# Kernel optimization log

Measured on AMD Instinct MI355X. Metric: run time of the kernel, lower is better.

Reference implementation:

```python
import jax, jax.numpy as jnp
import numpy as np

N = 100000      # nodes
D = 128         # input feature dim
K = 8           # propagation hops (concat K+1 blocks)
HID = 512
OUT = 32
E = 1600000     # edges (avg degree 16)
BN_EPS = 1e-5
DEG_EPS = 1e-8


def setup_inputs() -> dict:
    key = jax.random.key(0)
    ks = jax.random.split(key, 8)
    feature = jax.random.normal(ks[0], (N, D), dtype=jnp.float32)
    coor = jax.random.uniform(ks[1], (N, 2), dtype=jnp.float32)
    edge_index = jax.random.randint(ks[2], (2, E), 0, N, dtype=jnp.int32)
    theta = jnp.array(1.0, dtype=jnp.float32)  # Gaussian bandwidth param
    fan1 = D * (K + 1)
    W1 = jax.random.normal(ks[3], (HID, fan1), dtype=jnp.float32) * (1.0 / np.sqrt(fan1))
    b1 = jnp.zeros((HID,), dtype=jnp.float32)
    gamma = jnp.ones((HID,), dtype=jnp.float32)
    beta = jnp.zeros((HID,), dtype=jnp.float32)
    W2 = jax.random.normal(ks[4], (OUT, HID), dtype=jnp.float32) * (1.0 / np.sqrt(HID))
    b2 = jnp.zeros((OUT,), dtype=jnp.float32)
    return {"feature": feature, "coor": coor, "theta": theta,
            "W1": W1, "b1": b1, "gamma": gamma, "beta": beta,
            "W2": W2, "b2": b2, "edge_index": edge_index, "m": 1}


def reference(feature, coor, theta, W1, b1, gamma, beta, W2, b2, edge_index, m):
    row, col = edge_index[0], edge_index[1]  # dst, src
    # Gaussian kernel edge weights from coordinate distances (gather on coor)
    diff = coor[row] - coor[col]                       # [E, 2]
    dist2 = jnp.sum(diff * diff, axis=-1)              # [E]
    w = jnp.exp(-dist2 * theta / m)                    # [E]
    # degree (row) normalization via scatter-add
    deg = jax.ops.segment_sum(w, row, num_segments=N)  # [N]
    norm = w / (deg[row] + DEG_EPS)                    # [E]
    # K sequential propagations, concat with input (-> N x D*(K+1))
    xs = [feature]
    x = feature
    for _ in range(K):
        msgs = x[col] * norm[:, None]                  # [E, D] gather + weight
        x = jax.ops.segment_sum(msgs, row, num_segments=N)  # [N, D] scatter
        xs.append(x)
    h = jnp.concatenate(xs, axis=-1)                   # [N, D*(K+1)]
    # MLP head: fc1 -> leaky_relu(0.2) -> BatchNorm1d (batch stats) -> fc2
    h = jax.nn.leaky_relu(h @ W1.T + b1, negative_slope=0.2)
    mu = jnp.mean(h, axis=0)
    var = jnp.var(h, axis=0)
    h = (h - mu) * jax.lax.rsqrt(var + BN_EPS) * gamma + beta
    # dropout omitted (deterministic/eval reference)
    return h @ W2.T + b2
```

## Files before the change

### kernel.cpp

```cpp
#include <hip/hip_runtime.h>
#include <hip/hip_bf16.h>
#include <cstdint>
#include <cstddef>

#define NNODES 100000
#define DFEAT 128
#define KHOP 8
#define FAN1 1152
#define HIDN 512
#define OUTD 32
#define NEDGE 1600000
#define BN_EPS 1e-5f
#define DEG_EPS 1e-8f
#define FIXSCALE 67108864.0f

using short8 = __attribute__((ext_vector_type(8))) short;
using f32x4  = __attribute__((ext_vector_type(4))) float;

__device__ __forceinline__ float bf16lo(uint32_t u) { return __uint_as_float(u << 16); }
__device__ __forceinline__ float bf16hi(uint32_t u) { return __uint_as_float(u & 0xffff0000u); }
__device__ __forceinline__ float bf16s(short x) {
    return __uint_as_float(((uint32_t)(uint16_t)x) << 16);
}
__device__ __forceinline__ uint32_t packbf(float a, float b) {
    uint32_t lo = __bfloat16_as_ushort(__float2bfloat16(a));
    uint32_t hi = __bfloat16_as_ushort(__float2bfloat16(b));
    return lo | (hi << 16);
}

__device__ __forceinline__ void gload16(const void* g, void* l) {
    __builtin_amdgcn_global_load_lds(
        (const __attribute__((address_space(1))) uint32_t*)g,
        (__attribute__((address_space(3))) uint32_t*)l, 16, 0, 0);
}

struct Blk3 { const __hip_bfloat16* p[3]; };

__global__ __launch_bounds__(256) void edge_kernel(
    const int* __restrict__ ei, const float* __restrict__ coor,
    const float* __restrict__ theta, const int* __restrict__ mm,
    unsigned long long* __restrict__ packed, unsigned short* __restrict__ rank)
{
    int e = blockIdx.x * 256 + threadIdx.x;
    if (e >= NEDGE) return;
    float tom = theta[0] / (float)mm[0];
    int r = ei[e], c = ei[NEDGE + e];
    float2 pr = *(const float2*)(coor + 2*(size_t)r);
    float2 pc = *(const float2*)(coor + 2*(size_t)c);
    float dx = pr.x - pc.x, dy = pr.y - pc.y;
    float w = expf(-(dx*dx + dy*dy) * tom);
    unsigned long long enc = (1ULL << 48)
        | (unsigned long long)(unsigned int)__float2uint_rn(w * FIXSCALE);
    unsigned long long old = atomicAdd(&packed[r], enc);
    rank[e] = (unsigned short)(old >> 48);
}

__global__ __launch_bounds__(1024) void scan_local(
    const unsigned long long* __restrict__ packed, int* __restrict__ row_ptr,
    int* __restrict__ bsum, int n)
{
    __shared__ int wsum[16];
    int b = blockIdx.x, tid = threadIdx.x;
    int i = b * 1024 + tid;
    int lane = tid & 63, wv = tid >> 6;
    int v = (i < n) ? (int)(packed[i] >> 48) : 0;
    #pragma unroll
    for (int off = 1; off < 64; off <<= 1) {
        int t = __shfl_up(v, off, 64);
        if (lane >= off) v += t;
    }
    if (lane == 63) wsum[wv] = v;
    __syncthreads();
    if (tid < 16) {
        int t = wsum[tid];
        #pragma unroll
        for (int off = 1; off < 16; off <<= 1) {
            int u = __shfl_up(t, off, 64);
            if (tid >= off) t += u;
        }
        wsum[tid] = t;
    }
    __syncthreads();
    int incl = v + ((wv == 0) ? 0 : wsum[wv - 1]);
    if (i < n) row_ptr[i + 1] = incl;
    if (tid == 0) bsum[b] = wsum[15];
}

__global__ __launch_bounds__(128) void scan_carry(int* __restrict__ bsum, int n)
{
    __shared__ int ws[2];
    int tid = threadIdx.x, lane = tid & 63, wv = tid >> 6;
    int v = (tid < n) ? bsum[tid] : 0;
    int incl = v;
    #pragma unroll
    for (int off = 1; off < 64; off <<= 1) {
        int t = __shfl_up(incl, off, 64);
        if (lane >= off) incl += t;
    }
    if (lane == 63) ws[wv] = incl;
    __syncthreads();
    int excl = incl - v + ((wv == 0) ? 0 : ws[0]);
    if (tid < n) bsum[tid] = excl;
}

__global__ __launch_bounds__(256) void scan_add(
    const int* __restrict__ bsum, int* __restrict__ row_ptr, int n)
{
    int i = blockIdx.x * 256 + threadIdx.x;
    if (i == 0) row_ptr[0] = 0;
    if (i < n) row_ptr[i + 1] += bsum[i >> 10];
}

__global__ __launch_bounds__(256) void fill_kernel(
    const int* __restrict__ ei, const float* __restrict__ coor,
    const float* __restrict__ theta, const int* __restrict__ mm,
    const unsigned long long* __restrict__ packed,
    const unsigned short* __restrict__ rank, const int* __restrict__ row_ptr,
    uint2* __restrict__ edat)
{
    int e = blockIdx.x * 256 + threadIdx.x;
    if (e >= NEDGE) return;
    float tom = theta[0] / (float)mm[0];
    int r = ei[e], c = ei[NEDGE + e];
    float2 pr = *(const float2*)(coor + 2*(size_t)r);
    float2 pc = *(const float2*)(coor + 2*(size_t)c);
    float dx = pr.x - pc.x, dy = pr.y - pc.y;
    float w = expf(-(dx*dx + dy*dy) * tom);
    float deg = (float)(double)(packed[r] & 0xFFFFFFFFFFFFULL) * (1.0f / FIXSCALE);
    int pos = row_ptr[r] + rank[e];
    uint2 d;
    d.x = (unsigned)c;
    d.y = __float_as_uint(w / (deg + DEG_EPS));
    edat[pos] = d;
}

__global__ __launch_bounds__(256) void cast_feat_kernel(
    const float* __restrict__ f, __hip_bfloat16* __restrict__ x0)
{
    int i = blockIdx.x * 256 + threadIdx.x;
    int node = i >> 6, l2 = i & 63;
    if (node >= NNODES) return;
    float2 v = *(const float2*)(f + (size_t)node * DFEAT + l2 * 2);
    __hip_bfloat162 hb;
    hb.x = __float2bfloat16(v.x);
    hb.y = __float2bfloat16(v.y);
    *(__hip_bfloat162*)(x0 + (size_t)node * DFEAT + l2 * 2) = hb;
}

__global__ __launch_bounds__(256) void cast_w1_kernel(
    const float* __restrict__ w1, __hip_bfloat16* __restrict__ o)
{
    int i = blockIdx.x * 256 + threadIdx.x;
    if (i < HIDN * FAN1) o[i] = __float2bfloat16(w1[i]);
}

__global__ __launch_bounds__(256) void prop_kernel(
    const __hip_bfloat16* __restrict__ x, __hip_bfloat16* __restrict__ y,
    const int* __restrict__ row_ptr, const uint2* __restrict__ edat)
{
    int gw = (blockIdx.x * 256 + threadIdx.x) >> 6;
    if (gw >= NNODES) return;
    int lane = threadIdx.x & 63;
    int q = lane >> 4, sl = lane & 15;
    int beg = row_ptr[gw], end = row_ptr[gw + 1];
    float a0 = 0.f, a1 = 0.f, a2 = 0.f, a3 = 0.f;
    float a4 = 0.f, a5 = 0.f, a6 = 0.f, a7 = 0.f;
    int e = beg + q;
    for (; e + 12 < end; e += 16) {
        uint2 e0 = edat[e], e1 = edat[e + 4], e2 = edat[e + 8], e3 = edat[e + 12];
        float w0 = __uint_as_float(e0.y), w1 = __uint_as_float(e1.y);
        float w2 = __uint_as_float(e2.y), w3 = __uint_as_float(e3.y);
        uint4 u0 = *(const uint4*)(x + (size_t)e0.x * DFEAT + sl * 8);
        uint4 u1 = *(const uint4*)(x + (size_t)e1.x * DFEAT + sl * 8);
        uint4 u2 = *(const uint4*)(x + (size_t)e2.x * DFEAT + sl * 8);
        uint4 u3 = *(const uint4*)(x + (size_t)e3.x * DFEAT + sl * 8);
        a0 += w0 * bf16lo(u0.x); a1 += w0 * bf16hi(u0.x);
        a2 += w0 * bf16lo(u0.y); a3 += w0 * bf16hi(u0.y);
        a4 += w0 * bf16lo(u0.z); a5 += w0 * bf16hi(u0.z);
        a6 += w0 * bf16lo(u0.w); a7 += w0 * bf16hi(u0.w);
        a0 += w1 * bf16lo(u1.x); a1 += w1 * bf16hi(u1.x);
        a2 += w1 * bf16lo(u1.y); a3 += w1 * bf16hi(u1.y);
        a4 += w1 * bf16lo(u1.z); a5 += w1 * bf16hi(u1.z);
        a6 += w1 * bf16lo(u1.w); a7 += w1 * bf16hi(u1.w);
        a0 += w2 * bf16lo(u2.x); a1 += w2 * bf16hi(u2.x);
        a2 += w2 * bf16lo(u2.y); a3 += w2 * bf16hi(u2.y);
        a4 += w2 * bf16lo(u2.z); a5 += w2 * bf16hi(u2.z);
        a6 += w2 * bf16lo(u2.w); a7 += w2 * bf16hi(u2.w);
        a0 += w3 * bf16lo(u3.x); a1 += w3 * bf16hi(u3.x);
        a2 += w3 * bf16lo(u3.y); a3 += w3 * bf16hi(u3.y);
        a4 += w3 * bf16lo(u3.z); a5 += w3 * bf16hi(u3.z);
        a6 += w3 * bf16lo(u3.w); a7 += w3 * bf16hi(u3.w);
    }
    for (; e < end; e += 4) {
        uint2 e0 = edat[e];
        float w0 = __uint_as_float(e0.y);
        uint4 u0 = *(const uint4*)(x + (size_t)e0.x * DFEAT + sl * 8);
        a0 += w0 * bf16lo(u0.x); a1 += w0 * bf16hi(u0.x);
        a2 += w0 * bf16lo(u0.y); a3 += w0 * bf16hi(u0.y);
        a4 += w0 * bf16lo(u0.z); a5 += w0 * bf16hi(u0.z);
        a6 += w0 * bf16lo(u0.w); a7 += w0 * bf16hi(u0.w);
    }
    a0 += __shfl_xor(a0, 16, 64); a0 += __shfl_xor(a0, 32, 64);
    a1 += __shfl_xor(a1, 16, 64); a1 += __shfl_xor(a1, 32, 64);
    a2 += __shfl_xor(a2, 16, 64); a2 += __shfl_xor(a2, 32, 64);
    a3 += __shfl_xor(a3, 16, 64); a3 += __shfl_xor(a3, 32, 64);
    a4 += __shfl_xor(a4, 16, 64); a4 += __shfl_xor(a4, 32, 64);
    a5 += __shfl_xor(a5, 16, 64); a5 += __shfl_xor(a5, 32, 64);
    a6 += __shfl_xor(a6, 16, 64); a6 += __shfl_xor(a6, 32, 64);
    a7 += __shfl_xor(a7, 16, 64); a7 += __shfl_xor(a7, 32, 64);
    if (q == 0) {
        uint4 o;
        o.x = packbf(a0, a1);
        o.y = packbf(a2, a3);
        o.z = packbf(a4, a5);
        o.w = packbf(a6, a7);
        *(uint4*)(y + (size_t)gw * DFEAT + sl * 8) = o;
    }
}

__global__ __launch_bounds__(256) void fc1_kernel(
    Blk3 blks, const __hip_bfloat16* __restrict__ w1,
    const float* __restrict__ b1, __hip_bfloat16* __restrict__ h1b,
    float* __restrict__ gsum, float* __restrict__ gsq,
    int nkt, int kb0, int mode)
{
    __shared__ char smem[33792];
    int pid = blockIdx.x;
    int lid = (pid & 7) * 391 + (pid >> 3);
    int n0 = (lid & 3) * 128;
    int m0 = (lid >> 2) * 128;
    int tid = threadIdx.x, lane = tid & 63, wv = tid >> 6;
    int wr = wv >> 1, wc = wv & 1;

    f32x4 acc[4][4];
    #pragma unroll
    for (int i = 0; i < 4; ++i)
        #pragma unroll
        for (int j = 0; j < 4; ++j)
            acc[i][j] = (f32x4){0.f, 0.f, 0.f, 0.f};

#define STAGE(hb, ktv) do {                                                   \
        const __hip_bfloat16* xp = blks.p[(ktv) >> 2];                        \
        int koff_ = ((ktv) & 3) * 32;                                         \
        int kglob_ = (kb0 + ((ktv) >> 2)) * 128 + koff_;                      \
        char* Ab_ = smem + (hb) * 16384;                                      \
        char* Bb_ = Ab_ + 8192;                                               \
        _Pragma("unroll")                                                     \
        for (int l = 0; l < 2; ++l) {                                         \
            int u = l * 256 + wv * 64 + lane;                                 \
            int row_ = u >> 2, qq_ = u & 3;                                   \
            gload16(xp + (size_t)(m0 + row_) * DFEAT + koff_ + qq_ * 8,       \
                    Ab_ + u * 16);                                            \
            gload16(w1 + (size_t)(n0 + row_) * FAN1 + kglob_ + qq_ * 8,       \
                    Bb_ + u * 16);                                            \
        }                                                                     \
    } while (0)

    STAGE(0, 0);
    for (int kt = 0; kt < nkt; ++kt) {
        int cur = kt & 1;
        __builtin_amdgcn_s_barrier();
        if (kt + 1 < nkt) {
            STAGE(cur ^ 1, kt + 1);
            asm volatile("s_waitcnt vmcnt(4)" ::: "memory");
        } else {
            asm volatile("s_waitcnt vmcnt(0)" ::: "memory");
        }
        __builtin_amdgcn_s_barrier();
        char* Ab = smem + cur * 16384;
        char* Bb = Ab + 8192;
        short8 af[4], bfr[4];
        #pragma unroll
        for (int i = 0; i < 4; ++i)
            af[i] = *(const short8*)(Ab + (wr * 64 + i * 16 + (lane & 15)) * 64 + (lane >> 4) * 16);
        #pragma unroll
        for (int j = 0; j < 4; ++j)
            bfr[j] = *(const short8*)(Bb + (wc * 64 + j * 16 + (lane & 15)) * 64 + (lane >> 4) * 16);
        #pragma unroll
        for (int j = 0; j < 4; ++j)
            #pragma unroll
            for (int i = 0; i < 4; ++i)
                acc[i][j] = __builtin_amdgcn_mfma_f32_16x16x32_bf16(af[i], bfr[j], acc[i][j], 0, 0, 0);
    }
#undef STAGE

    __syncthreads();
    __hip_bfloat16* tile = (__hip_bfloat16*)smem;
    float* lsum = (float*)(smem + 32768);
    float* lsq  = lsum + 128;
    bool fin = (mode & 2) != 0;
    if (fin && tid < 128) { lsum[tid] = 0.f; lsq[tid] = 0.f; }
    #pragma unroll
    for (int i = 0; i < 4; ++i) {
        #pragma unroll
        for (int j = 0; j < 4; ++j) {
            int col = wc * 64 + j * 16 + (lane & 15);
            #pragma unroll
            for (int r = 0; r < 4; ++r) {
                int row = wr * 64 + i * 16 + (lane >> 4) * 4 + r;
                tile[row * 128 + col] = __float2bfloat16(acc[i][j][r]);
            }
        }
    }
    __syncthreads();

    int cu = tid & 15, tr = tid >> 4;
    float bias[8];
    float s[8], q[8];
    #pragma unroll
    for (int e = 0; e < 8; ++e) { s[e] = 0.f; q[e] = 0.f; }
    if (fin) {
        #pragma unroll
        for (int e = 0; e < 8; ++e) bias[e] = b1[n0 + cu * 8 + e];
    }
    size_t blkbase = (size_t)(n0 >> 7) * NNODES * 128;
    for (int p = 0; p < 8; ++p) {
        int row = p * 16 + tr;
        int gm = m0 + row;
        if (gm >= NNODES) continue;
        short8 fresh = *(const short8*)(tile + row * 128 + cu * 8);
        size_t gidx = blkbase + (size_t)gm * 128 + cu * 8;
        float v[8];
        #pragma unroll
        for (int e = 0; e < 8; ++e) v[e] = bf16s(fresh[e]);
        if (mode & 1) {
            short8 prev = *(const short8*)(h1b + gidx);
            #pragma unroll
            for (int e = 0; e < 8; ++e) v[e] += bf16s(prev[e]);
        }
        if (fin) {
            #pragma unroll
            for (int e = 0; e < 8; ++e) {
                float t = v[e] + bias[e];
                t = (t > 0.f) ? t : 0.2f * t;
                v[e] = t;
                s[e] += t;
                q[e] += t * t;
            }
        }
        short8 outv;
        #pragma unroll
        for (int e = 0; e < 8; ++e) outv[e] = (short)__bfloat16_as_ushort(__float2bfloat16(v[e]));
        *(short8*)(h1b + gidx) = outv;
    }
    if (fin) {
        #pragma unroll
        for (int e = 0; e < 8; ++e) {
            atomicAdd(&lsum[cu * 8 + e], s[e]);
            atomicAdd(&lsq[cu * 8 + e], q[e]);
        }
        __syncthreads();
        if (tid < 128) {
            atomicAdd(&gsum[n0 + tid], lsum[tid]);
            atomicAdd(&gsq[n0 + tid], lsq[tid]);
        }
    }
}

__global__ __launch_bounds__(512) void bn_finalize(
    const float* __restrict__ gsum, const float* __restrict__ gsq,
    const float* __restrict__ gamma, const float* __restrict__ beta,
    const float* __restrict__ w2, const float* __restrict__ b2,
    __hip_bfloat16* __restrict__ w2s, float* __restrict__ cvec)
{
    __shared__ float ts[HIDN];
    int tid = threadIdx.x;
    float mu = gsum[tid] * (1.0f / NNODES);
    float var = gsq[tid] * (1.0f / NNODES) - mu * mu;
    float s = gamma[tid] * rsqrtf(var + BN_EPS);
    float t = beta[tid] - mu * s;
    ts[tid] = t;
    for (int o = 0; o < OUTD; ++o)
        w2s[o * HIDN + tid] = __float2bfloat16(w2[o * HIDN + tid] * s);
    __syncthreads();
    int lane = tid & 63, wv = tid >> 6;
    for (int o = wv; o < OUTD; o += 8) {
        float p = 0.f;
        for (int j = lane; j < HIDN; j += 64) p += ts[j] * w2[o * HIDN + j];
        #pragma unroll
        for (int off = 32; off; off >>= 1) p += __shfl_xor(p, off, 64);
        if (lane == 0) cvec[o] = p + b2[o];
    }
}

__global__ __launch_bounds__(256) void fc2_kernel(
    const __hip_bfloat16* __restrict__ h1b, const __hip_bfloat16* __restrict__ w2s,
    const float* __restrict__ cvec, float* __restrict__ out)
{
    int gw = (blockIdx.x * 256 + threadIdx.x) >> 6;
    if (gw >= NNODES / 16) return;
    int lane = threadIdx.x & 63;
    int m0 = gw * 16;
    f32x4 acc[2];
    acc[0] = (f32x4){0.f, 0.f, 0.f, 0.f};
    acc[1] = (f32x4){0.f, 0.f, 0.f, 0.f};
    #pragma unroll
    for (int kt = 0; kt < HIDN / 32; ++kt) {
        int k0 = kt * 32;
        short8 a = *(const short8*)(h1b
            + ((size_t)(kt >> 2) * NNODES + (m0 + (lane & 15))) * 128
            + (kt & 3) * 32 + (lane >> 4) * 8);
        #pragma unroll
        for (int j = 0; j < 2; ++j) {
            short8 b = *(const short8*)(w2s + (size_t)(j * 16 + (lane & 15)) * HIDN + k0 + (lane >> 4) * 8);
            acc[j] = __builtin_amdgcn_mfma_f32_16x16x32_bf16(a, b, acc[j], 0, 0, 0);
        }
    }
    #pragma unroll
    for (int j = 0; j < 2; ++j) {
        int col = j * 16 + (lane & 15);
        float cadd = cvec[col];
        #pragma unroll
        for (int r = 0; r < 4; ++r) {
            int row = m0 + (lane >> 4) * 4 + r;
            out[(size_t)row * OUTD + col] = acc[j][r] + cadd;
        }
    }
}

struct Ptrs {
    float *gsum, *gsq, *cvec;
    int *row_ptr, *bsum;
    unsigned long long* packed;
    unsigned short* rank;
    uint2* edat;
    __hip_bfloat16 *slot[3], *h1acc, *w1b, *w2s;
};

static size_t layout(char* base, Ptrs& P) {
    char* p = base;
    auto take = [&](size_t b) {
        char* q = (char*)(((uintptr_t)p + 255) & ~(uintptr_t)255);
        p = q + b;
        return q;
    };
    P.packed  = (unsigned long long*)take((size_t)NNODES * 8);
    P.rank    = (unsigned short*)take((size_t)NEDGE * 2);
    P.row_ptr = (int*)  take((size_t)(NNODES + 1) * 4);
    P.bsum    = (int*)  take(128 * 4);
    P.edat    = (uint2*)take((size_t)NEDGE * 8);
    P.h1acc   = (__hip_bfloat16*)take((size_t)NNODES * HIDN * 2 + 65536);
    P.w1b     = (__hip_bfloat16*)take((size_t)HIDN * FAN1 * 2);
    P.w2s     = (__hip_bfloat16*)take((size_t)OUTD * HIDN * 2);
    P.gsum    = (float*)take(HIDN * 4);
    P.gsq     = (float*)take(HIDN * 4);
    P.cvec    = (float*)take(OUTD * 4);
    for (int i = 0; i < 3; ++i)
        P.slot[i] = (__hip_bfloat16*)take((size_t)NNODES * DFEAT * 2 + 32768);
    return (size_t)(p - base);
}

extern "C" void kernel_launch(void* const* d_in, const int* in_sizes, int n_in,
                              void* d_out, int out_size, void* d_ws, size_t ws_size,
                              hipStream_t stream)
{
    const float* feature = (const float*)d_in[0];
    const float* coor    = (const float*)d_in[1];
    const float* theta   = (const float*)d_in[2];
    const float* W1      = (const float*)d_in[3];
    const float* b1      = (const float*)d_in[4];
    const float* gamma   = (const float*)d_in[5];
    const float* beta    = (const float*)d_in[6];
    const float* W2      = (const float*)d_in[7];
    const float* b2      = (const float*)d_in[8];
    const int*   ei      = (const int*)d_in[9];
    const int*   mm      = (const int*)d_in[10];
    float* out = (float*)d_out;
    (void)in_sizes; (void)n_in; (void)out_size; (void)ws_size;

    Ptrs P;
    layout((char*)d_ws, P);

    hipMemsetAsync(P.packed, 0, (size_t)NNODES * 8, stream);
    hipMemsetAsync(P.gsum,   0, HIDN * 4, stream);
    hipMemsetAsync(P.gsq,    0, HIDN * 4, stream);

    int eb = (NEDGE + 255) / 256;
    int nchunk = (NNODES + 1023) / 1024;
    edge_kernel<<<eb, 256, 0, stream>>>(ei, coor, theta, mm, P.packed, P.rank);
    scan_local<<<nchunk, 1024, 0, stream>>>(P.packed, P.row_ptr, P.bsum, NNODES);
    scan_carry<<<1, 128, 0, stream>>>(P.bsum, nchunk);
    scan_add<<<(NNODES + 255) / 256, 256, 0, stream>>>(P.bsum, P.row_ptr, NNODES);
    fill_kernel<<<eb, 256, 0, stream>>>(ei, coor, theta, mm, P.packed, P.rank,
                                        P.row_ptr, P.edat);

    cast_w1_kernel<<<(HIDN * FAN1 + 255) / 256, 256, 0, stream>>>(W1, P.w1b);
    cast_feat_kernel<<<(NNODES * 64) / 256, 256, 0, stream>>>(feature, P.slot[0]);

    int pb = (NNODES * 64) / 256;
    int fgrid = 8 * 391;

    auto launch_fc1 = [&](int kb0, int mode) {
        Blk3 b;
        for (int i = 0; i < 3; ++i) b.p[i] = P.slot[i];
        fc1_kernel<<<fgrid, 256, 0, stream>>>(b, P.w1b, b1, P.h1acc,
                                              P.gsum, P.gsq, 12, kb0, mode);
    };

    for (int k = 1; k <= KHOP; ++k) {
        prop_kernel<<<pb, 256, 0, stream>>>(P.slot[(k - 1) % 3],
                                            P.slot[k % 3],
                                            P.row_ptr, P.edat);
        if (k == 2) launch_fc1(0, 0);
        if (k == 5) launch_fc1(3, 1);
    }
    launch_fc1(6, 3);

    bn_finalize<<<1, 512, 0, stream>>>(P.gsum, P.gsq, gamma, beta, W2, b2,
                                       P.w2s, P.cvec);
    fc2_kernel<<<(NNODES / 16 * 64 + 255) / 256, 256, 0, stream>>>(P.h1acc, P.w2s,
                                                                   P.cvec, out);
}
```

Measured before the change: 924.1 us.

## Swizzle fc1 LDS tiles and use nontemporal loads for streamed edge and hidden data

In fc1, global-to-LDS staging now permutes the 16-byte chunk within each 64-byte row by an XOR swizzle, and the MFMA fragment reads apply the matching permutation to reduce LDS bank conflicts. The propagation kernel reads packed edge (src, weight) records as 64-bit nontemporal loads, and fc2 reads hidden activations with nontemporal loads. The nontemporal hints are meant to keep single-use streams from evicting the reused feature rows from cache. The swizzle has to match exactly between writer and reader, or the matrix multiply gives wrong results.

```diff
diff --git a/kernel.cpp b/kernel.cpp
--- a/kernel.cpp
+++ b/kernel.cpp
@@ -16,6 +16,7 @@
 
 using short8 = __attribute__((ext_vector_type(8))) short;
 using f32x4  = __attribute__((ext_vector_type(4))) float;
+using u32x4  = __attribute__((ext_vector_type(4))) unsigned int;
 
 __device__ __forceinline__ float bf16lo(uint32_t u) { return __uint_as_float(u << 16); }
 __device__ __forceinline__ float bf16hi(uint32_t u) { return __uint_as_float(u & 0xffff0000u); }
@@ -165,15 +166,21 @@
     int beg = row_ptr[gw], end = row_ptr[gw + 1];
     float a0 = 0.f, a1 = 0.f, a2 = 0.f, a3 = 0.f;
     float a4 = 0.f, a5 = 0.f, a6 = 0.f, a7 = 0.f;
+    const unsigned long long* ed64 = (const unsigned long long*)edat;
     int e = beg + q;
     for (; e + 12 < end; e += 16) {
-        uint2 e0 = edat[e], e1 = edat[e + 4], e2 = edat[e + 8], e3 = edat[e + 12];
-        float w0 = __uint_as_float(e0.y), w1 = __uint_as_float(e1.y);
-        float w2 = __uint_as_float(e2.y), w3 = __uint_as_float(e3.y);
-        uint4 u0 = *(const uint4*)(x + (size_t)e0.x * DFEAT + sl * 8);
-        uint4 u1 = *(const uint4*)(x + (size_t)e1.x * DFEAT + sl * 8);
-        uint4 u2 = *(const uint4*)(x + (size_t)e2.x * DFEAT + sl * 8);
-        uint4 u3 = *(const uint4*)(x + (size_t)e3.x * DFEAT + sl * 8);
+        unsigned long long d0 = __builtin_nontemporal_load(ed64 + e);
+        unsigned long long d1 = __builtin_nontemporal_load(ed64 + e + 4);
+        unsigned long long d2 = __builtin_nontemporal_load(ed64 + e + 8);
+        unsigned long long d3 = __builtin_nontemporal_load(ed64 + e + 12);
+        float w0 = __uint_as_float((unsigned)(d0 >> 32));
+        float w1 = __uint_as_float((unsigned)(d1 >> 32));
+        float w2 = __uint_as_float((unsigned)(d2 >> 32));
+        float w3 = __uint_as_float((unsigned)(d3 >> 32));
+        uint4 u0 = *(const uint4*)(x + (size_t)(unsigned)d0 * DFEAT + sl * 8);
+        uint4 u1 = *(const uint4*)(x + (size_t)(unsigned)d1 * DFEAT + sl * 8);
+        uint4 u2 = *(const uint4*)(x + (size_t)(unsigned)d2 * DFEAT + sl * 8);
+        uint4 u3 = *(const uint4*)(x + (size_t)(unsigned)d3 * DFEAT + sl * 8);
         a0 += w0 * bf16lo(u0.x); a1 += w0 * bf16hi(u0.x);
         a2 += w0 * bf16lo(u0.y); a3 += w0 * bf16hi(u0.y);
         a4 += w0 * bf16lo(u0.z); a5 += w0 * bf16hi(u0.z);
@@ -192,9 +199,9 @@
         a6 += w3 * bf16lo(u3.w); a7 += w3 * bf16hi(u3.w);
     }
     for (; e < end; e += 4) {
-        uint2 e0 = edat[e];
-        float w0 = __uint_as_float(e0.y);
-        uint4 u0 = *(const uint4*)(x + (size_t)e0.x * DFEAT + sl * 8);
+        unsigned long long d0 = __builtin_nontemporal_load(ed64 + e);
+        float w0 = __uint_as_float((unsigned)(d0 >> 32));
+        uint4 u0 = *(const uint4*)(x + (size_t)(unsigned)d0 * DFEAT + sl * 8);
         a0 += w0 * bf16lo(u0.x); a1 += w0 * bf16hi(u0.x);
         a2 += w0 * bf16lo(u0.y); a3 += w0 * bf16hi(u0.y);
         a4 += w0 * bf16lo(u0.z); a5 += w0 * bf16hi(u0.z);
@@ -231,6 +238,8 @@
     int m0 = (lid >> 2) * 128;
     int tid = threadIdx.x, lane = tid & 63, wv = tid >> 6;
     int wr = wv >> 1, wc = wv & 1;
+    int sq = (lane & 3) ^ ((lane >> 3) & 3);
+    int rch = (lane >> 4) ^ (((lane & 15) >> 1) & 3);
 
     f32x4 acc[4][4];
     #pragma unroll
@@ -248,10 +257,10 @@
         _Pragma("unroll")                                                     \
         for (int l = 0; l < 2; ++l) {                                         \
             int u = l * 256 + wv * 64 + lane;                                 \
-            int row_ = u >> 2, qq_ = u & 3;                                   \
-            gload16(xp + (size_t)(m0 + row_) * DFEAT + koff_ + qq_ * 8,       \
+            int row_ = u >> 2;                                                \
+            gload16(xp + (size_t)(m0 + row_) * DFEAT + koff_ + sq * 8,        \
                     Ab_ + u * 16);                                            \
-            gload16(w1 + (size_t)(n0 + row_) * FAN1 + kglob_ + qq_ * 8,       \
+            gload16(w1 + (size_t)(n0 + row_) * FAN1 + kglob_ + sq * 8,        \
                     Bb_ + u * 16);                                            \
         }                                                                     \
     } while (0)
@@ -272,10 +281,10 @@
         short8 af[4], bfr[4];
         #pragma unroll
         for (int i = 0; i < 4; ++i)
-            af[i] = *(const short8*)(Ab + (wr * 64 + i * 16 + (lane & 15)) * 64 + (lane >> 4) * 16);
+            af[i] = *(const short8*)(Ab + (wr * 64 + i * 16 + (lane & 15)) * 64 + rch * 16);
         #pragma unroll
         for (int j = 0; j < 4; ++j)
-            bfr[j] = *(const short8*)(Bb + (wc * 64 + j * 16 + (lane & 15)) * 64 + (lane >> 4) * 16);
+            bfr[j] = *(const short8*)(Bb + (wc * 64 + j * 16 + (lane & 15)) * 64 + rch * 16);
         #pragma unroll
         for (int j = 0; j < 4; ++j)
             #pragma unroll
@@ -397,9 +406,12 @@
     #pragma unroll
     for (int kt = 0; kt < HIDN / 32; ++kt) {
         int k0 = kt * 32;
-        short8 a = *(const short8*)(h1b
+        const u32x4* ap = (const u32x4*)(h1b
             + ((size_t)(kt >> 2) * NNODES + (m0 + (lane & 15))) * 128
             + (kt & 3) * 32 + (lane >> 4) * 8);
+        u32x4 araw = __builtin_nontemporal_load(ap);
+        short8 a;
+        *(u32x4*)&a = araw;
         #pragma unroll
         for (int j = 0; j < 2; ++j) {
             short8 b = *(const short8*)(w2s + (size_t)(j * 16 + (lane & 15)) * HIDN + k0 + (lane >> 4) * 8);
```

Result: slower. 973.7 us (+5.4%).
